# Kernel tuning notes

Hardware: AMD Instinct MI355X
Metric: run time of the kernel (lower is better)

## Reference

```python
import jax, jax.numpy as jnp
import numpy as np

B, N, C, H = 8, 16384, 256, 128
FG_NPOINT = 4096
SAMPLE_POINT = 1024
MAX_TRANSLATE = jnp.array([3.0, 3.0, 2.0], dtype=jnp.float32)


def _fps(xyz, n_sample):
    # xyz: [N,3] -> indices [n_sample] (D-FPS, seed index 0)
    d0 = jnp.sum((xyz - xyz[0]) ** 2, axis=-1)  # [N]

    def body(dists, _):
        idx = jnp.argmax(dists)
        d = jnp.sum((xyz - xyz[idx]) ** 2, axis=-1)
        return jnp.minimum(dists, d), idx

    _, idxs = jax.lax.scan(body, d0, None, length=n_sample - 1)
    return jnp.concatenate([jnp.zeros((1,), dtype=idxs.dtype), idxs])


def fps_batch(xyz, n_sample):
    return jax.vmap(lambda p: _fps(p, n_sample))(xyz)  # [B, n_sample]


def gather_pts(xyz, idx):
    # xyz [B,N,3], idx [B,S] -> [B,S,3]
    return jnp.take_along_axis(xyz, idx[..., None], axis=1)


def gather_feat(feat, idx):
    # feat [B,C,N], idx [B,S] -> [B,C,S]
    return jnp.take_along_axis(feat, idx[:, None, :], axis=2)


def setup_inputs() -> dict:
    key = jax.random.key(0)
    ks = jax.random.split(key, 6)
    return {
        "xyz": jax.random.normal(ks[0], (B, N, 3), jnp.float32) * 10.0,
        "features": jax.random.normal(ks[1], (B, C, N), jnp.float32),
        "seg_w1": jax.random.normal(ks[2], (H, C), jnp.float32) * 0.05,
        "seg_scale1": jnp.ones((H,), jnp.float32),
        "seg_bias1": jnp.zeros((H,), jnp.float32),
        "seg_w2": jax.random.normal(ks[3], (1, H), jnp.float32) * 0.05,
        "seg_b2": jnp.zeros((1,), jnp.float32),
        "vote_w1": jax.random.normal(ks[4], (H, C), jnp.float32) * 0.05,
        "vote_scale1": jnp.ones((H,), jnp.float32),
        "vote_bias1": jnp.zeros((H,), jnp.float32),
        "reg_w": jax.random.normal(ks[5], (3, H), jnp.float32) * 0.05,
        "reg_b": jnp.zeros((3,), jnp.float32),
    }


def reference(xyz, features, seg_w1, seg_scale1, seg_bias1, seg_w2, seg_b2,
              vote_w1, vote_scale1, vote_bias1, reg_w, reg_b):
    # ---- seg branch: 1x1 conv + BN(eval affine) + ReLU, then 1x1 conv to num_class
    h = jax.nn.relu(jnp.einsum('oc,bcn->bon', seg_w1, features)
                    * seg_scale1[None, :, None] + seg_bias1[None, :, None])
    seg = jnp.einsum('oc,bon->bcn'.replace('c', 'k'), seg_w2, h)  # [B,1,N]
    seg = seg + seg_b2[None, :, None]
    seg_score = jax.nn.sigmoid(jnp.max(seg, axis=1))  # [B,N] (max over class dim)

    # ---- top-k foreground selection
    _, fg_idx = jax.lax.top_k(seg_score, FG_NPOINT)  # [B,M]
    fg_xyz = gather_pts(xyz, fg_idx)                  # [B,M,3]
    fg_feat = gather_feat(features, fg_idx)           # [B,C,M]

    # ---- vote/offset layer (3DSSD-style): MLP -> clamped offset
    vh = jax.nn.relu(jnp.einsum('oc,bcm->bom', vote_w1, fg_feat)
                     * vote_scale1[None, :, None] + vote_bias1[None, :, None])  # [B,H,M]
    reg = jnp.einsum('oh,bhm->bom', reg_w, vh) + reg_b[None, :, None]  # [B,3,M]
    offset = jnp.clip(reg.transpose(0, 2, 1), -MAX_TRANSLATE, MAX_TRANSLATE)  # [B,M,3]
    fg_xyz_ctr = fg_xyz + offset
    fg_feat_ctr = vh

    # ---- original-point FPS sampler + gathers
    ori_idx = fps_batch(fg_xyz, SAMPLE_POINT)
    sampled_ori_xyz = gather_pts(fg_xyz, ori_idx)
    sampled_ori_feat = gather_feat(fg_feat, ori_idx)

    # ---- center-point FPS sampler + gathers
    ctr_idx = fps_batch(fg_xyz_ctr, SAMPLE_POINT)
    sampled_ctr_xyz = gather_pts(fg_xyz_ctr, ctr_idx)
    sampled_ctr_feat = gather_feat(fg_feat_ctr, ctr_idx)
    sampled_ctr_offset = gather_pts(offset, ctr_idx)
    sampled_ctr_origin = gather_pts(fg_xyz, ctr_idx)

    # ---- aggregation concat (USE_ORIGINAL_POINT=True)
    agg_xyz = jnp.concatenate([sampled_ctr_xyz, sampled_ori_xyz], axis=1)       # [B,2S,3]
    agg_feat = jnp.concatenate([sampled_ctr_feat, sampled_ori_feat[:, :H, :]], axis=-1)  # [B,H,2S]

    return (agg_xyz, agg_feat, sampled_ctr_xyz, sampled_ctr_offset,
            sampled_ctr_origin, seg)
```

## Files before the change

kernel.cpp:

```cpp
#include <hip/hip_runtime.h>

#define NB 8
#define NP 16384
#define NC 256
#define NH 128
#define NM 4096
#define NS 1024

typedef float v2f __attribute__((ext_vector_type(2)));

__device__ __forceinline__ unsigned long long make_key(float v, int n) {
  unsigned u = __float_as_uint(v);
  u = (u & 0x80000000u) ? ~u : (u | 0x80000000u);
  unsigned d = ~u;
  return (((unsigned long long)d) << 32) | (unsigned)n;
}

__device__ __forceinline__ float wave_max_dpp(float v) {
#define DPPMAX(ctrl)                                                            \
  v = fmaxf(v, __int_as_float(__builtin_amdgcn_update_dpp(                      \
                 __float_as_int(v), __float_as_int(v), (ctrl), 0xf, 0xf, false)))
  DPPMAX(0xB1);
  DPPMAX(0x4E);
  DPPMAX(0x141);
  DPPMAX(0x140);
  DPPMAX(0x142);
  DPPMAX(0x143);
#undef DPPMAX
  return __int_as_float(__builtin_amdgcn_readlane(__float_as_int(v), 63));
}

template <int CTRL>
__device__ __forceinline__ unsigned long long dpp64(unsigned long long v) {
  int lo = (int)(unsigned)v, hi = (int)(unsigned)(v >> 32);
  lo = __builtin_amdgcn_update_dpp(lo, lo, CTRL, 0xf, 0xf, false);
  hi = __builtin_amdgcn_update_dpp(hi, hi, CTRL, 0xf, 0xf, false);
  return (((unsigned long long)(unsigned)hi) << 32) | (unsigned)lo;
}

__global__ __launch_bounds__(256) void transpose_w_kernel(
    const float* __restrict__ wseg, const float* __restrict__ wvote,
    float* __restrict__ tseg, float* __restrict__ tvote) {
  int i = blockIdx.x * 256 + threadIdx.x;
  int c = i >> 7, o = i & 127;
  tseg[i] = wseg[o * NC + c];
  tvote[i] = wvote[o * NC + c];
}

__global__ __launch_bounds__(256) void seg_kernel(
    const float* __restrict__ features, const float* __restrict__ w1t,
    const float* __restrict__ scale1, const float* __restrict__ bias1,
    const float* __restrict__ w2, const float* __restrict__ b2,
    float* __restrict__ seg_out, unsigned long long* __restrict__ keys) {
  __shared__ float wt[32][128];
  __shared__ float ft[32][64];
  __shared__ float red[16][64];
  __shared__ float Ssh[64];
  __shared__ float w2sh[128];
  int b = blockIdx.y;
  int n0 = blockIdx.x * 64;
  int tid = threadIdx.x;
  int lane = tid & 63;
  int ro = tid >> 4, rc = tid & 15;
  float a0 = w2[lane], a1 = w2[lane + 64];
  float whi = fmaxf(a0, a1), wlo = fminf(a0, a1);
#pragma unroll
  for (int off = 32; off >= 1; off >>= 1) {
    whi = fmaxf(whi, __shfl_xor(whi, off, 64));
    wlo = fminf(wlo, __shfl_xor(wlo, off, 64));
  }
  if (tid < 128) w2sh[tid] = w2[tid];
  const float* fb = features + (size_t)b * NC * NP;
  float acc[8][4] = {};
  for (int kc = 0; kc < NC; kc += 32) {
    for (int q = tid; q < 4096; q += 256) {
      int kk = q >> 7, o = q & 127;
      wt[kk][o] = w1t[(kc + kk) * NH + o];
    }
    for (int q = tid; q < 2048; q += 256) {
      int kk = q >> 6, nn = q & 63;
      ft[kk][nn] = fb[(size_t)(kc + kk) * NP + n0 + nn];
    }
    __syncthreads();
#pragma unroll
    for (int kk = 0; kk < 32; ++kk) {
      float wv[8], fv[4];
#pragma unroll
      for (int i = 0; i < 8; ++i) wv[i] = wt[kk][ro * 8 + i];
#pragma unroll
      for (int j = 0; j < 4; ++j) fv[j] = ft[kk][rc * 4 + j];
#pragma unroll
      for (int i = 0; i < 8; ++i)
#pragma unroll
        for (int j = 0; j < 4; ++j) acc[i][j] = fmaf(wv[i], fv[j], acc[i][j]);
    }
    __syncthreads();
  }
  float part[4] = {};
#pragma unroll
  for (int i = 0; i < 8; ++i) {
    int o = ro * 8 + i;
    float sc = scale1[o], bi = bias1[o];
#pragma unroll
    for (int j = 0; j < 4; ++j) {
      float h = fmaxf(fmaf(acc[i][j], sc, bi), 0.0f);
      part[j] += h;
    }
  }
#pragma unroll
  for (int j = 0; j < 4; ++j) red[ro][rc * 4 + j] = part[j];
  __syncthreads();
  float b2v = b2[0];
  if (tid < 64) {
    float S = 0.0f;
#pragma unroll
    for (int r = 0; r < 16; ++r) S += red[r][tid];
    Ssh[tid] = S;
    float m = (S >= 0.0f ? whi * S : wlo * S) + b2v;
    float sig = 1.0f / (1.0f + expf(-m));
    int nn = n0 + tid;
    keys[(size_t)b * NP + nn] = make_key(sig, nn);
  }
  __syncthreads();
  int n = tid & 63, kg = tid >> 6;
  float S = Ssh[n];
  size_t base = ((size_t)b * 128 + (size_t)kg * 32) * NP + n0 + n;
#pragma unroll
  for (int kk = 0; kk < 32; ++kk)
    seg_out[base + (size_t)kk * NP] = fmaf(w2sh[kg * 32 + kk], S, b2v);
}

__global__ __launch_bounds__(1024) void sort8k_kernel(unsigned long long* __restrict__ keys) {
  __shared__ unsigned long long sk[8192];
  int chunk = blockIdx.x & 1, b = blockIdx.x >> 1;
  bool desc = (chunk == 1);
  unsigned long long* K = keys + (size_t)b * NP + chunk * 8192;
  int tid = threadIdx.x;
  for (int i = tid; i < 8192; i += 1024) sk[i] = K[i];
  __syncthreads();
  for (int k = 2; k <= 8192; k <<= 1) {
    for (int j = k >> 1; j > 0; j >>= 1) {
      for (int i = tid; i < 8192; i += 1024) {
        int ixj = i ^ j;
        if (ixj > i) {
          bool up = (((i & k) == 0) != desc);
          unsigned long long a = sk[i], c = sk[ixj];
          if ((a > c) == up) { sk[i] = c; sk[ixj] = a; }
        }
      }
      __syncthreads();
    }
  }
  for (int i = tid; i < 8192; i += 1024) K[i] = sk[i];
}

__global__ __launch_bounds__(1024) void merge_topk_kernel(
    const unsigned long long* __restrict__ keys, int* __restrict__ fg_idx,
    float* __restrict__ fg_xyz, const float* __restrict__ xyz) {
  __shared__ unsigned long long sk[8192];
  int b = blockIdx.x;
  const unsigned long long* K = keys + (size_t)b * NP;
  int tid = threadIdx.x;
  for (int i = tid; i < 8192; i += 1024) {
    unsigned long long a = K[i], c = K[i + 8192];
    sk[i] = (a < c) ? a : c;
  }
  __syncthreads();
  for (int j = 4096; j > 0; j >>= 1) {
    for (int i = tid; i < 8192; i += 1024) {
      int ixj = i ^ j;
      if (ixj > i) {
        unsigned long long a = sk[i], c = sk[ixj];
        if (a > c) { sk[i] = c; sk[ixj] = a; }
      }
    }
    __syncthreads();
  }
  for (int m = tid; m < NM; m += 1024) {
    unsigned long long key = sk[m];
    int idx = (int)(key & 0xffffffffULL);
    fg_idx[b * NM + m] = idx;
    size_t src = ((size_t)b * NP + idx) * 3;
    size_t dst = ((size_t)b * NM + m) * 3;
    fg_xyz[dst + 0] = xyz[src + 0];
    fg_xyz[dst + 1] = xyz[src + 1];
    fg_xyz[dst + 2] = xyz[src + 2];
  }
}

__global__ __launch_bounds__(256) void vote_kernel(
    const float* __restrict__ features, const int* __restrict__ fg_idx,
    const float* __restrict__ w1t, const float* __restrict__ scale1,
    const float* __restrict__ bias1, const float* __restrict__ rw,
    const float* __restrict__ rb, const float* __restrict__ fg_xyz,
    float* __restrict__ vh, float* __restrict__ offs, float* __restrict__ fg_ctr) {
  __shared__ float wt[32][128];
  __shared__ float ft[32][64];
  __shared__ float hl[128][65];
  __shared__ int idx_l[64];
  int b = blockIdx.y;
  int m0 = blockIdx.x * 64;
  int tid = threadIdx.x;
  int ro = tid >> 4, rc = tid & 15;
  const float* fb = features + (size_t)b * NC * NP;
  if (tid < 64) idx_l[tid] = fg_idx[b * NM + m0 + tid];
  __syncthreads();
  float acc[8][4] = {};
  for (int kc = 0; kc < NC; kc += 32) {
    for (int q = tid; q < 4096; q += 256) {
      int kk = q >> 7, o = q & 127;
      wt[kk][o] = w1t[(kc + kk) * NH + o];
    }
    for (int q = tid; q < 2048; q += 256) {
      int kk = q >> 6, mm = q & 63;
      ft[kk][mm] = fb[(size_t)(kc + kk) * NP + idx_l[mm]];
    }
    __syncthreads();
#pragma unroll
    for (int kk = 0; kk < 32; ++kk) {
      float wv[8], fv[4];
#pragma unroll
      for (int i = 0; i < 8; ++i) wv[i] = wt[kk][ro * 8 + i];
#pragma unroll
      for (int j = 0; j < 4; ++j) fv[j] = ft[kk][rc * 4 + j];
#pragma unroll
      for (int i = 0; i < 8; ++i)
#pragma unroll
        for (int j = 0; j < 4; ++j) acc[i][j] = fmaf(wv[i], fv[j], acc[i][j]);
    }
    __syncthreads();
  }
#pragma unroll
  for (int i = 0; i < 8; ++i) {
    int o = ro * 8 + i;
    float sc = scale1[o], bi = bias1[o];
#pragma unroll
    for (int j = 0; j < 4; ++j) {
      float h = fmaxf(fmaf(acc[i][j], sc, bi), 0.0f);
      hl[o][rc * 4 + j] = h;
      vh[((size_t)b * NH + o) * NM + m0 + rc * 4 + j] = h;
    }
  }
  __syncthreads();
  if (tid < 64) {
    int m = m0 + tid;
    const float MT[3] = {3.0f, 3.0f, 2.0f};
#pragma unroll
    for (int r = 0; r < 3; ++r) {
      float a = 0.0f;
      for (int o = 0; o < NH; ++o) a = fmaf(rw[r * NH + o], hl[o][tid], a);
      a += rb[r];
      a = fminf(fmaxf(a, -MT[r]), MT[r]);
      size_t p = ((size_t)b * NM + m) * 3 + r;
      offs[p] = a;
      fg_ctr[p] = __fadd_rn(fg_xyz[p], a);
    }
  }
}

#define PPT 8
__global__ __launch_bounds__(512) void fps_kernel(
    const float* __restrict__ fg_xyz, const float* __restrict__ fg_ctr,
    int* __restrict__ ori_idx, int* __restrict__ ctr_idx) {
#pragma clang fp contract(off)
  __shared__ float4 pts[NM];
  __shared__ unsigned long long wkey[2][8];
  __shared__ int sel_list[NS];
  int set = blockIdx.x & 1, b = blockIdx.x >> 1;
  const float* P = (set == 0 ? fg_xyz : fg_ctr) + (size_t)b * NM * 3;
  int* O = (set == 0 ? ori_idx : ctr_idx) + b * NS;
  int tid = threadIdx.x;
  for (int m = tid; m < NM; m += 512)
    pts[m] = make_float4(P[m * 3 + 0], P[m * 3 + 1], P[m * 3 + 2], 0.0f);
  __syncthreads();
  v2f x2[4], y2[4], z2[4], d2[4];
#pragma unroll
  for (int j = 0; j < 4; ++j) {
    float4 pa = pts[tid * PPT + 2 * j];
    float4 pb = pts[tid * PPT + 2 * j + 1];
    v2f t;
    t.x = pa.x; t.y = pb.x; x2[j] = t;
    t.x = pa.y; t.y = pb.y; y2[j] = t;
    t.x = pa.z; t.y = pb.z; z2[j] = t;
    t.x = 3.402823466e38f; t.y = 3.402823466e38f; d2[j] = t;
  }
  if (tid == 0) sel_list[0] = 0;
  int lane = tid & 63, wave = tid >> 6;
  int base_idx = tid * PPT;
  float sx = pts[0].x, sy = pts[0].y, sz = pts[0].z;
  for (int it = 1; it < NS; ++it) {
    v2f sxv, syv, szv;
    sxv.x = sx; sxv.y = sx;
    syv.x = sy; syv.y = sy;
    szv.x = sz; szv.y = sz;
    float bd = -1.0f;
    int bc = 0;
#pragma unroll
    for (int j = 0; j < 4; ++j) {
      v2f dx = x2[j] - sxv, dy = y2[j] - syv, dz = z2[j] - szv;
      v2f dd = (dx * dx + dy * dy) + dz * dz;
      v2f nd;
      nd.x = fminf(d2[j].x, dd.x);
      nd.y = fminf(d2[j].y, dd.y);
      d2[j] = nd;
      if (j == 0) {
        bd = nd.x; bc = base_idx;
        bool g = nd.y > bd; bd = g ? nd.y : bd; bc = g ? base_idx + 1 : bc;
      } else {
        bool g0 = nd.x > bd; bd = g0 ? nd.x : bd; bc = g0 ? base_idx + 2 * j : bc;
        bool g1 = nd.y > bd; bd = g1 ? nd.y : bd; bc = g1 ? base_idx + 2 * j + 1 : bc;
      }
    }
    float wm = wave_max_dpp(bd);
    unsigned long long msk = __ballot(bd == wm);
    int wl = __ffsll((long long)msk) - 1;
    if (lane == wl)
      wkey[it & 1][wave] =
          (((unsigned long long)__float_as_uint(bd)) << 32) | (unsigned)(4095 - bc);
    __syncthreads();
    unsigned long long k = wkey[it & 1][lane & 7];
    { unsigned long long o = dpp64<0xB1>(k);  if (o > k) k = o; }
    { unsigned long long o = dpp64<0x4E>(k);  if (o > k) k = o; }
    { unsigned long long o = dpp64<0x141>(k); if (o > k) k = o; }
    int sel = 4095 - (int)(k & 0xffffffffULL);
    if (tid == 0) sel_list[it] = sel;
    float4 s = pts[sel];
    sx = s.x; sy = s.y; sz = s.z;
  }
  __syncthreads();
  for (int s2 = tid; s2 < NS; s2 += 512) O[s2] = sel_list[s2];
}

__global__ __launch_bounds__(256) void feat_out_kernel(
    const float* __restrict__ vh, const float* __restrict__ features,
    const int* __restrict__ fg_idx, const int* __restrict__ ori_idx,
    const int* __restrict__ ctr_idx, float* __restrict__ out_feat) {
  int b = blockIdx.z;
  int o = blockIdx.y * 4 + (threadIdx.x >> 6);
  int s = blockIdx.x * 64 + (threadIdx.x & 63);
  float val;
  if (s < NS) {
    int i = ctr_idx[b * NS + s];
    val = vh[((size_t)b * NH + o) * NM + i];
  } else {
    int i = ori_idx[b * NS + (s - NS)];
    int g = fg_idx[b * NM + i];
    val = features[((size_t)b * NC + o) * NP + g];
  }
  out_feat[((size_t)b * NH + o) * (2 * NS) + s] = val;
}

__global__ __launch_bounds__(256) void xyz_out_kernel(
    const float* __restrict__ fg_xyz, const float* __restrict__ fg_ctr,
    const float* __restrict__ offs, const int* __restrict__ ori_idx,
    const int* __restrict__ ctr_idx, float* __restrict__ out_agg,
    float* __restrict__ out_cxyz, float* __restrict__ out_coff,
    float* __restrict__ out_corg) {
  int b = blockIdx.y;
  int s = blockIdx.x * 256 + threadIdx.x;
  if (s < NS) {
    int i = ctr_idx[b * NS + s];
    size_t src = ((size_t)b * NM + i) * 3;
    size_t d_agg = ((size_t)b * 2 * NS + s) * 3;
    size_t d_s = ((size_t)b * NS + s) * 3;
#pragma unroll
    for (int r = 0; r < 3; ++r) {
      float c = fg_ctr[src + r];
      out_agg[d_agg + r] = c;
      out_cxyz[d_s + r] = c;
      out_coff[d_s + r] = offs[src + r];
      out_corg[d_s + r] = fg_xyz[src + r];
    }
  } else {
    int i = ori_idx[b * NS + (s - NS)];
    size_t src = ((size_t)b * NM + i) * 3;
    size_t d_agg = ((size_t)b * 2 * NS + s) * 3;
#pragma unroll
    for (int r = 0; r < 3; ++r) out_agg[d_agg + r] = fg_xyz[src + r];
  }
}

extern "C" void kernel_launch(void* const* d_in, const int* in_sizes, int n_in,
                              void* d_out, int out_size, void* d_ws, size_t ws_size,
                              hipStream_t stream) {
  const float* xyz = (const float*)d_in[0];
  const float* features = (const float*)d_in[1];
  const float* seg_w1 = (const float*)d_in[2];
  const float* seg_scale1 = (const float*)d_in[3];
  const float* seg_bias1 = (const float*)d_in[4];
  const float* seg_w2 = (const float*)d_in[5];
  const float* seg_b2 = (const float*)d_in[6];
  const float* vote_w1 = (const float*)d_in[7];
  const float* vote_scale1 = (const float*)d_in[8];
  const float* vote_bias1 = (const float*)d_in[9];
  const float* reg_w = (const float*)d_in[10];
  const float* reg_b = (const float*)d_in[11];
  float* out = (float*)d_out;

  char* ws = (char*)d_ws;
  unsigned long long* keys = (unsigned long long*)(ws + 0);
  int* fg_idx = (int*)(ws + 1048576);
  float* fg_xyz = (float*)(ws + 1179648);
  float* fg_ctr = (float*)(ws + 1572864);
  float* offs = (float*)(ws + 1966080);
  int* ori_idx = (int*)(ws + 2359296);
  int* ctr_idx = (int*)(ws + 2392064);
  float* vh = (float*)(ws + 2424832);
  float* w1t_s = (float*)(ws + 19202048);
  float* w1t_v = (float*)(ws + 19333120);

  float* out_agg_xyz = out;
  float* out_agg_feat = out + 49152;
  float* out_ctr_xyz = out + 2146304;
  float* out_ctr_off = out + 2170880;
  float* out_ctr_org = out + 2195456;
  float* out_seg = out + 2220032;

  transpose_w_kernel<<<128, 256, 0, stream>>>(seg_w1, vote_w1, w1t_s, w1t_v);
  seg_kernel<<<dim3(NP / 64, NB), 256, 0, stream>>>(
      features, w1t_s, seg_scale1, seg_bias1, seg_w2, seg_b2, out_seg, keys);
  sort8k_kernel<<<2 * NB, 1024, 0, stream>>>(keys);
  merge_topk_kernel<<<NB, 1024, 0, stream>>>(keys, fg_idx, fg_xyz, xyz);
  vote_kernel<<<dim3(NM / 64, NB), 256, 0, stream>>>(
      features, fg_idx, w1t_v, vote_scale1, vote_bias1, reg_w, reg_b, fg_xyz,
      vh, offs, fg_ctr);
  fps_kernel<<<16, 512, 0, stream>>>(fg_xyz, fg_ctr, ori_idx, ctr_idx);
  feat_out_kernel<<<dim3(32, 32, NB), 256, 0, stream>>>(
      vh, features, fg_idx, ori_idx, ctr_idx, out_agg_feat);
  xyz_out_kernel<<<dim3(8, NB), 256, 0, stream>>>(
      fg_xyz, fg_ctr, offs, ori_idx, ctr_idx, out_agg_xyz, out_ctr_xyz,
      out_ctr_off, out_ctr_org);
}
```

Baseline: 1.083 ms.

## Fuse both FPS samplers per batch into one block sharing barriers

The FPS kernel now runs the original-point and center-point samplers for one batch inside a single block, interleaving the two per-iteration updates so they share one __syncthreads per iteration. This halves the block count (8 instead of 16) and amortizes barrier and reduction latency across two independent chains. Point storage moves from float4 AoS to SoA arrays, and indices are written directly to global instead of buffered in shared memory. It doubles per-thread register use and leaves more of the GPU idle, so the serial per-iteration cost must drop enough to compensate.

```diff
diff --git a/kernel.cpp b/kernel.cpp
--- a/kernel.cpp
+++ b/kernel.cpp
@@ -259,76 +259,103 @@
 }
 
 #define PPT 8
+__device__ __forceinline__ void fps_update8(
+    const v2f* x, const v2f* y, const v2f* z, v2f* d,
+    float sx, float sy, float sz, int base_idx, float& bd, int& bc) {
+#pragma clang fp contract(off)
+  v2f sxv, syv, szv;
+  sxv.x = sx; sxv.y = sx;
+  syv.x = sy; syv.y = sy;
+  szv.x = sz; szv.y = sz;
+  bd = -1.0f;
+  bc = base_idx;
+#pragma unroll
+  for (int j = 0; j < 4; ++j) {
+    v2f dx = x[j] - sxv, dy = y[j] - syv, dz = z[j] - szv;
+    v2f dd = (dx * dx + dy * dy) + dz * dz;
+    v2f nd;
+    nd.x = fminf(d[j].x, dd.x);
+    nd.y = fminf(d[j].y, dd.y);
+    d[j] = nd;
+    if (j == 0) {
+      bd = nd.x; bc = base_idx;
+      bool g = nd.y > bd; bd = g ? nd.y : bd; bc = g ? base_idx + 1 : bc;
+    } else {
+      bool g0 = nd.x > bd; bd = g0 ? nd.x : bd; bc = g0 ? base_idx + 2 * j : bc;
+      bool g1 = nd.y > bd; bd = g1 ? nd.y : bd; bc = g1 ? base_idx + 2 * j + 1 : bc;
+    }
+  }
+}
+
 __global__ __launch_bounds__(512) void fps_kernel(
     const float* __restrict__ fg_xyz, const float* __restrict__ fg_ctr,
     int* __restrict__ ori_idx, int* __restrict__ ctr_idx) {
 #pragma clang fp contract(off)
-  __shared__ float4 pts[NM];
-  __shared__ unsigned long long wkey[2][8];
-  __shared__ int sel_list[NS];
-  int set = blockIdx.x & 1, b = blockIdx.x >> 1;
-  const float* P = (set == 0 ? fg_xyz : fg_ctr) + (size_t)b * NM * 3;
-  int* O = (set == 0 ? ori_idx : ctr_idx) + b * NS;
+  __shared__ float pxA[NM], pyA[NM], pzA[NM];
+  __shared__ float pxB[NM], pyB[NM], pzB[NM];
+  __shared__ unsigned long long wkeyA[2][8], wkeyB[2][8];
+  int b = blockIdx.x;
+  const float* PA = fg_xyz + (size_t)b * NM * 3;
+  const float* PB = fg_ctr + (size_t)b * NM * 3;
+  int* OA = ori_idx + b * NS;
+  int* OB = ctr_idx + b * NS;
   int tid = threadIdx.x;
-  for (int m = tid; m < NM; m += 512)
-    pts[m] = make_float4(P[m * 3 + 0], P[m * 3 + 1], P[m * 3 + 2], 0.0f);
-  __syncthreads();
-  v2f x2[4], y2[4], z2[4], d2[4];
+  for (int m = tid; m < NM; m += 512) {
+    pxA[m] = PA[m * 3 + 0]; pyA[m] = PA[m * 3 + 1]; pzA[m] = PA[m * 3 + 2];
+    pxB[m] = PB[m * 3 + 0]; pyB[m] = PB[m * 3 + 1]; pzB[m] = PB[m * 3 + 2];
+  }
+  __syncthreads();
+  v2f xA[4], yA[4], zA[4], dA[4], xB[4], yB[4], zB[4], dB[4];
+  int base_idx = tid * PPT;
 #pragma unroll
   for (int j = 0; j < 4; ++j) {
-    float4 pa = pts[tid * PPT + 2 * j];
-    float4 pb = pts[tid * PPT + 2 * j + 1];
+    int m0 = base_idx + 2 * j, m1 = m0 + 1;
     v2f t;
-    t.x = pa.x; t.y = pb.x; x2[j] = t;
-    t.x = pa.y; t.y = pb.y; y2[j] = t;
-    t.x = pa.z; t.y = pb.z; z2[j] = t;
-    t.x = 3.402823466e38f; t.y = 3.402823466e38f; d2[j] = t;
-  }
-  if (tid == 0) sel_list[0] = 0;
+    t.x = pxA[m0]; t.y = pxA[m1]; xA[j] = t;
+    t.x = pyA[m0]; t.y = pyA[m1]; yA[j] = t;
+    t.x = pzA[m0]; t.y = pzA[m1]; zA[j] = t;
+    t.x = pxB[m0]; t.y = pxB[m1]; xB[j] = t;
+    t.x = pyB[m0]; t.y = pyB[m1]; yB[j] = t;
+    t.x = pzB[m0]; t.y = pzB[m1]; zB[j] = t;
+    t.x = 3.402823466e38f; t.y = 3.402823466e38f;
+    dA[j] = t; dB[j] = t;
+  }
+  if (tid == 0) { OA[0] = 0; OB[0] = 0; }
   int lane = tid & 63, wave = tid >> 6;
-  int base_idx = tid * PPT;
-  float sx = pts[0].x, sy = pts[0].y, sz = pts[0].z;
+  float sxA = pxA[0], syA = pyA[0], szA = pzA[0];
+  float sxB = pxB[0], syB = pyB[0], szB = pzB[0];
   for (int it = 1; it < NS; ++it) {
-    v2f sxv, syv, szv;
-    sxv.x = sx; sxv.y = sx;
-    syv.x = sy; syv.y = sy;
-    szv.x = sz; szv.y = sz;
-    float bd = -1.0f;
-    int bc = 0;
-#pragma unroll
-    for (int j = 0; j < 4; ++j) {
-      v2f dx = x2[j] - sxv, dy = y2[j] - syv, dz = z2[j] - szv;
-      v2f dd = (dx * dx + dy * dy) + dz * dz;
-      v2f nd;
-      nd.x = fminf(d2[j].x, dd.x);
-      nd.y = fminf(d2[j].y, dd.y);
-      d2[j] = nd;
-      if (j == 0) {
-        bd = nd.x; bc = base_idx;
-        bool g = nd.y > bd; bd = g ? nd.y : bd; bc = g ? base_idx + 1 : bc;
-      } else {
-        bool g0 = nd.x > bd; bd = g0 ? nd.x : bd; bc = g0 ? base_idx + 2 * j : bc;
-        bool g1 = nd.y > bd; bd = g1 ? nd.y : bd; bc = g1 ? base_idx + 2 * j + 1 : bc;
-      }
-    }
-    float wm = wave_max_dpp(bd);
-    unsigned long long msk = __ballot(bd == wm);
-    int wl = __ffsll((long long)msk) - 1;
-    if (lane == wl)
-      wkey[it & 1][wave] =
-          (((unsigned long long)__float_as_uint(bd)) << 32) | (unsigned)(4095 - bc);
-    __syncthreads();
-    unsigned long long k = wkey[it & 1][lane & 7];
-    { unsigned long long o = dpp64<0xB1>(k);  if (o > k) k = o; }
-    { unsigned long long o = dpp64<0x4E>(k);  if (o > k) k = o; }
-    { unsigned long long o = dpp64<0x141>(k); if (o > k) k = o; }
-    int sel = 4095 - (int)(k & 0xffffffffULL);
-    if (tid == 0) sel_list[it] = sel;
-    float4 s = pts[sel];
-    sx = s.x; sy = s.y; sz = s.z;
-  }
-  __syncthreads();
-  for (int s2 = tid; s2 < NS; s2 += 512) O[s2] = sel_list[s2];
+    float bdA; int bcA;
+    fps_update8(xA, yA, zA, dA, sxA, syA, szA, base_idx, bdA, bcA);
+    float wmA = wave_max_dpp(bdA);
+    unsigned long long mA = __ballot(bdA == wmA);
+    int wlA = __ffsll((long long)mA) - 1;
+    if (lane == wlA)
+      wkeyA[it & 1][wave] =
+          (((unsigned long long)__float_as_uint(bdA)) << 32) | (unsigned)(4095 - bcA);
+    float bdB; int bcB;
+    fps_update8(xB, yB, zB, dB, sxB, syB, szB, base_idx, bdB, bcB);
+    float wmB = wave_max_dpp(bdB);
+    unsigned long long mB = __ballot(bdB == wmB);
+    int wlB = __ffsll((long long)mB) - 1;
+    if (lane == wlB)
+      wkeyB[it & 1][wave] =
+          (((unsigned long long)__float_as_uint(bdB)) << 32) | (unsigned)(4095 - bcB);
+    __syncthreads();
+    unsigned long long kA = wkeyA[it & 1][lane & 7];
+    unsigned long long kB = wkeyB[it & 1][lane & 7];
+    { unsigned long long o = dpp64<0xB1>(kA);  if (o > kA) kA = o; }
+    { unsigned long long o = dpp64<0xB1>(kB);  if (o > kB) kB = o; }
+    { unsigned long long o = dpp64<0x4E>(kA);  if (o > kA) kA = o; }
+    { unsigned long long o = dpp64<0x4E>(kB);  if (o > kB) kB = o; }
+    { unsigned long long o = dpp64<0x141>(kA); if (o > kA) kA = o; }
+    { unsigned long long o = dpp64<0x141>(kB); if (o > kB) kB = o; }
+    int selA = 4095 - (int)(kA & 0xffffffffULL);
+    int selB = 4095 - (int)(kB & 0xffffffffULL);
+    if (tid == 0) { OA[it] = selA; OB[it] = selB; }
+    sxA = pxA[selA]; syA = pyA[selA]; szA = pzA[selA];
+    sxB = pxB[selB]; syB = pyB[selB]; szB = pzB[selB];
+  }
 }
 
 __global__ __launch_bounds__(256) void feat_out_kernel(
@@ -424,7 +451,7 @@
   vote_kernel<<<dim3(NM / 64, NB), 256, 0, stream>>>(
       features, fg_idx, w1t_v, vote_scale1, vote_bias1, reg_w, reg_b, fg_xyz,
       vh, offs, fg_ctr);
-  fps_kernel<<<16, 512, 0, stream>>>(fg_xyz, fg_ctr, ori_idx, ctr_idx);
+  fps_kernel<<<NB, 512, 0, stream>>>(fg_xyz, fg_ctr, ori_idx, ctr_idx);
   feat_out_kernel<<<dim3(32, 32, NB), 256, 0, stream>>>(
       vh, features, fg_idx, ori_idx, ctr_idx, out_agg_feat);
   xyz_out_kernel<<<dim3(8, NB), 256, 0, stream>>>(
```

New measurement: 1.531 ms. +41.4%, slower.

## Merge both FPS samplers per batch into one 1024-thread block with SoA LDS

Applied to the files above, without the earlier changes.

Each block now runs the original-point and center-point FPS for one batch at once, using two 512-thread groups that share a single barrier per iteration, instead of launching 16 separate 512-thread blocks. Point coordinates move from float4 AoS to SoA shared arrays, and the selected indices go straight to global memory rather than through a shared list. This halves the block count and combines the per-iteration barrier traffic. The risk is that 1024-thread barriers are slower than 512-thread ones and that 8 blocks use fewer CUs.

```diff
diff --git a/kernel.cpp b/kernel.cpp
--- a/kernel.cpp
+++ b/kernel.cpp
@@ -259,76 +259,85 @@
 }
 
 #define PPT 8
-__global__ __launch_bounds__(512) void fps_kernel(
+__device__ __forceinline__ void fps_update8(
+    const v2f* x, const v2f* y, const v2f* z, v2f* d,
+    float sx, float sy, float sz, int base_idx, float& bd, int& bc) {
+#pragma clang fp contract(off)
+  v2f sxv, syv, szv;
+  sxv.x = sx; sxv.y = sx;
+  syv.x = sy; syv.y = sy;
+  szv.x = sz; szv.y = sz;
+  bd = -1.0f;
+  bc = base_idx;
+#pragma unroll
+  for (int j = 0; j < 4; ++j) {
+    v2f dx = x[j] - sxv, dy = y[j] - syv, dz = z[j] - szv;
+    v2f dd = (dx * dx + dy * dy) + dz * dz;
+    v2f nd;
+    nd.x = fminf(d[j].x, dd.x);
+    nd.y = fminf(d[j].y, dd.y);
+    d[j] = nd;
+    if (j == 0) {
+      bd = nd.x; bc = base_idx;
+      bool g = nd.y > bd; bd = g ? nd.y : bd; bc = g ? base_idx + 1 : bc;
+    } else {
+      bool g0 = nd.x > bd; bd = g0 ? nd.x : bd; bc = g0 ? base_idx + 2 * j : bc;
+      bool g1 = nd.y > bd; bd = g1 ? nd.y : bd; bc = g1 ? base_idx + 2 * j + 1 : bc;
+    }
+  }
+}
+
+__global__ __launch_bounds__(1024) void fps_kernel(
     const float* __restrict__ fg_xyz, const float* __restrict__ fg_ctr,
     int* __restrict__ ori_idx, int* __restrict__ ctr_idx) {
 #pragma clang fp contract(off)
-  __shared__ float4 pts[NM];
-  __shared__ unsigned long long wkey[2][8];
-  __shared__ int sel_list[NS];
-  int set = blockIdx.x & 1, b = blockIdx.x >> 1;
-  const float* P = (set == 0 ? fg_xyz : fg_ctr) + (size_t)b * NM * 3;
-  int* O = (set == 0 ? ori_idx : ctr_idx) + b * NS;
+  __shared__ float px[2][NM], py[2][NM], pz[2][NM];
+  __shared__ unsigned long long wkey[2][2][8];
+  int b = blockIdx.x;
   int tid = threadIdx.x;
-  for (int m = tid; m < NM; m += 512)
-    pts[m] = make_float4(P[m * 3 + 0], P[m * 3 + 1], P[m * 3 + 2], 0.0f);
+  int grp = tid >> 9;
+  int ltid = tid & 511;
+  const float* P = (grp == 0 ? fg_xyz : fg_ctr) + (size_t)b * NM * 3;
+  int* O = (grp == 0 ? ori_idx : ctr_idx) + b * NS;
+  for (int m = ltid; m < NM; m += 512) {
+    px[grp][m] = P[m * 3 + 0];
+    py[grp][m] = P[m * 3 + 1];
+    pz[grp][m] = P[m * 3 + 2];
+  }
   __syncthreads();
   v2f x2[4], y2[4], z2[4], d2[4];
+  int base_idx = ltid * PPT;
 #pragma unroll
   for (int j = 0; j < 4; ++j) {
-    float4 pa = pts[tid * PPT + 2 * j];
-    float4 pb = pts[tid * PPT + 2 * j + 1];
+    int m0 = base_idx + 2 * j, m1 = m0 + 1;
     v2f t;
-    t.x = pa.x; t.y = pb.x; x2[j] = t;
-    t.x = pa.y; t.y = pb.y; y2[j] = t;
-    t.x = pa.z; t.y = pb.z; z2[j] = t;
-    t.x = 3.402823466e38f; t.y = 3.402823466e38f; d2[j] = t;
-  }
-  if (tid == 0) sel_list[0] = 0;
-  int lane = tid & 63, wave = tid >> 6;
-  int base_idx = tid * PPT;
-  float sx = pts[0].x, sy = pts[0].y, sz = pts[0].z;
+    t.x = px[grp][m0]; t.y = px[grp][m1]; x2[j] = t;
+    t.x = py[grp][m0]; t.y = py[grp][m1]; y2[j] = t;
+    t.x = pz[grp][m0]; t.y = pz[grp][m1]; z2[j] = t;
+    t.x = 3.402823466e38f; t.y = 3.402823466e38f;
+    d2[j] = t;
+  }
+  if (ltid == 0) O[0] = 0;
+  int lane = tid & 63, gwave = (tid >> 6) & 7;
+  float sx = px[grp][0], sy = py[grp][0], sz = pz[grp][0];
   for (int it = 1; it < NS; ++it) {
-    v2f sxv, syv, szv;
-    sxv.x = sx; sxv.y = sx;
-    syv.x = sy; syv.y = sy;
-    szv.x = sz; szv.y = sz;
-    float bd = -1.0f;
-    int bc = 0;
-#pragma unroll
-    for (int j = 0; j < 4; ++j) {
-      v2f dx = x2[j] - sxv, dy = y2[j] - syv, dz = z2[j] - szv;
-      v2f dd = (dx * dx + dy * dy) + dz * dz;
-      v2f nd;
-      nd.x = fminf(d2[j].x, dd.x);
-      nd.y = fminf(d2[j].y, dd.y);
-      d2[j] = nd;
-      if (j == 0) {
-        bd = nd.x; bc = base_idx;
-        bool g = nd.y > bd; bd = g ? nd.y : bd; bc = g ? base_idx + 1 : bc;
-      } else {
-        bool g0 = nd.x > bd; bd = g0 ? nd.x : bd; bc = g0 ? base_idx + 2 * j : bc;
-        bool g1 = nd.y > bd; bd = g1 ? nd.y : bd; bc = g1 ? base_idx + 2 * j + 1 : bc;
-      }
-    }
+    float bd; int bc;
+    fps_update8(x2, y2, z2, d2, sx, sy, sz, base_idx, bd, bc);
     float wm = wave_max_dpp(bd);
     unsigned long long msk = __ballot(bd == wm);
     int wl = __ffsll((long long)msk) - 1;
     if (lane == wl)
-      wkey[it & 1][wave] =
+      wkey[grp][it & 1][gwave] =
           (((unsigned long long)__float_as_uint(bd)) << 32) | (unsigned)(4095 - bc);
     __syncthreads();
-    unsigned long long k = wkey[it & 1][lane & 7];
+    unsigned long long k = wkey[grp][it & 1][lane & 7];
     { unsigned long long o = dpp64<0xB1>(k);  if (o > k) k = o; }
     { unsigned long long o = dpp64<0x4E>(k);  if (o > k) k = o; }
     { unsigned long long o = dpp64<0x141>(k); if (o > k) k = o; }
     int sel = 4095 - (int)(k & 0xffffffffULL);
-    if (tid == 0) sel_list[it] = sel;
-    float4 s = pts[sel];
-    sx = s.x; sy = s.y; sz = s.z;
-  }
-  __syncthreads();
-  for (int s2 = tid; s2 < NS; s2 += 512) O[s2] = sel_list[s2];
+    if (ltid == 0) O[it] = sel;
+    sx = px[grp][sel]; sy = py[grp][sel]; sz = pz[grp][sel];
+  }
 }
 
 __global__ __launch_bounds__(256) void feat_out_kernel(
@@ -424,7 +433,7 @@
   vote_kernel<<<dim3(NM / 64, NB), 256, 0, stream>>>(
       features, fg_idx, w1t_v, vote_scale1, vote_bias1, reg_w, reg_b, fg_xyz,
       vh, offs, fg_ctr);
-  fps_kernel<<<16, 512, 0, stream>>>(fg_xyz, fg_ctr, ori_idx, ctr_idx);
+  fps_kernel<<<NB, 1024, 0, stream>>>(fg_xyz, fg_ctr, ori_idx, ctr_idx);
   feat_out_kernel<<<dim3(32, 32, NB), 256, 0, stream>>>(
       vh, features, fg_idx, ori_idx, ctr_idx, out_agg_feat);
   xyz_out_kernel<<<dim3(8, NB), 256, 0, stream>>>(
```

Result: slower. 1.430 ms (+32.0%).

## Halve FPS block to four waves, 16 points per thread, simpler cross-wave reduction

Applied to the files above, without the earlier changes.

The FPS kernel now runs 256 threads per block instead of 512, with each thread holding 16 points in registers. The cross-wave argmax becomes two 128-bit shared loads plus scalar max compares, replacing the DPP shuffle over 8 wave keys. Point storage moves from float4 AoS to separate x/y/z arrays in shared memory. The aim is to cut barrier and reduction latency in the serial 1023-iteration loop, at the cost of twice the per-thread distance work and higher register pressure.

```diff
diff --git a/kernel.cpp b/kernel.cpp
--- a/kernel.cpp
+++ b/kernel.cpp
@@ -28,14 +28,6 @@
   DPPMAX(0x143);
 #undef DPPMAX
   return __int_as_float(__builtin_amdgcn_readlane(__float_as_int(v), 63));
-}
-
-template <int CTRL>
-__device__ __forceinline__ unsigned long long dpp64(unsigned long long v) {
-  int lo = (int)(unsigned)v, hi = (int)(unsigned)(v >> 32);
-  lo = __builtin_amdgcn_update_dpp(lo, lo, CTRL, 0xf, 0xf, false);
-  hi = __builtin_amdgcn_update_dpp(hi, hi, CTRL, 0xf, 0xf, false);
-  return (((unsigned long long)(unsigned)hi) << 32) | (unsigned)lo;
 }
 
 __global__ __launch_bounds__(256) void transpose_w_kernel(
@@ -258,45 +250,48 @@
   }
 }
 
-#define PPT 8
-__global__ __launch_bounds__(512) void fps_kernel(
+#define PPT 16
+__global__ __launch_bounds__(256) void fps_kernel(
     const float* __restrict__ fg_xyz, const float* __restrict__ fg_ctr,
     int* __restrict__ ori_idx, int* __restrict__ ctr_idx) {
 #pragma clang fp contract(off)
-  __shared__ float4 pts[NM];
-  __shared__ unsigned long long wkey[2][8];
+  __shared__ float px[NM], py[NM], pz[NM];
+  __shared__ __align__(32) unsigned long long wkey[2][4];
   __shared__ int sel_list[NS];
   int set = blockIdx.x & 1, b = blockIdx.x >> 1;
   const float* P = (set == 0 ? fg_xyz : fg_ctr) + (size_t)b * NM * 3;
   int* O = (set == 0 ? ori_idx : ctr_idx) + b * NS;
   int tid = threadIdx.x;
-  for (int m = tid; m < NM; m += 512)
-    pts[m] = make_float4(P[m * 3 + 0], P[m * 3 + 1], P[m * 3 + 2], 0.0f);
-  __syncthreads();
-  v2f x2[4], y2[4], z2[4], d2[4];
-#pragma unroll
-  for (int j = 0; j < 4; ++j) {
-    float4 pa = pts[tid * PPT + 2 * j];
-    float4 pb = pts[tid * PPT + 2 * j + 1];
+  for (int m = tid; m < NM; m += 256) {
+    px[m] = P[m * 3 + 0];
+    py[m] = P[m * 3 + 1];
+    pz[m] = P[m * 3 + 2];
+  }
+  __syncthreads();
+  v2f x2[8], y2[8], z2[8], d2[8];
+  int base_idx = tid * PPT;
+#pragma unroll
+  for (int j = 0; j < 8; ++j) {
+    int m0 = base_idx + 2 * j, m1 = m0 + 1;
     v2f t;
-    t.x = pa.x; t.y = pb.x; x2[j] = t;
-    t.x = pa.y; t.y = pb.y; y2[j] = t;
-    t.x = pa.z; t.y = pb.z; z2[j] = t;
-    t.x = 3.402823466e38f; t.y = 3.402823466e38f; d2[j] = t;
+    t.x = px[m0]; t.y = px[m1]; x2[j] = t;
+    t.x = py[m0]; t.y = py[m1]; y2[j] = t;
+    t.x = pz[m0]; t.y = pz[m1]; z2[j] = t;
+    t.x = 3.402823466e38f; t.y = 3.402823466e38f;
+    d2[j] = t;
   }
   if (tid == 0) sel_list[0] = 0;
   int lane = tid & 63, wave = tid >> 6;
-  int base_idx = tid * PPT;
-  float sx = pts[0].x, sy = pts[0].y, sz = pts[0].z;
+  float sx = px[0], sy = py[0], sz = pz[0];
   for (int it = 1; it < NS; ++it) {
     v2f sxv, syv, szv;
     sxv.x = sx; sxv.y = sx;
     syv.x = sy; syv.y = sy;
     szv.x = sz; szv.y = sz;
     float bd = -1.0f;
-    int bc = 0;
-#pragma unroll
-    for (int j = 0; j < 4; ++j) {
+    int bc = base_idx;
+#pragma unroll
+    for (int j = 0; j < 8; ++j) {
       v2f dx = x2[j] - sxv, dy = y2[j] - syv, dz = z2[j] - szv;
       v2f dd = (dx * dx + dy * dy) + dz * dz;
       v2f nd;
@@ -318,17 +313,17 @@
       wkey[it & 1][wave] =
           (((unsigned long long)__float_as_uint(bd)) << 32) | (unsigned)(4095 - bc);
     __syncthreads();
-    unsigned long long k = wkey[it & 1][lane & 7];
-    { unsigned long long o = dpp64<0xB1>(k);  if (o > k) k = o; }
-    { unsigned long long o = dpp64<0x4E>(k);  if (o > k) k = o; }
-    { unsigned long long o = dpp64<0x141>(k); if (o > k) k = o; }
-    int sel = 4095 - (int)(k & 0xffffffffULL);
+    const ulonglong2* wk = (const ulonglong2*)&wkey[it & 1][0];
+    ulonglong2 q0 = wk[0], q1 = wk[1];
+    unsigned long long m0 = q0.x > q0.y ? q0.x : q0.y;
+    unsigned long long m1 = q1.x > q1.y ? q1.x : q1.y;
+    unsigned long long km = m0 > m1 ? m0 : m1;
+    int sel = 4095 - (int)(km & 0xffffffffULL);
     if (tid == 0) sel_list[it] = sel;
-    float4 s = pts[sel];
-    sx = s.x; sy = s.y; sz = s.z;
-  }
-  __syncthreads();
-  for (int s2 = tid; s2 < NS; s2 += 512) O[s2] = sel_list[s2];
+    sx = px[sel]; sy = py[sel]; sz = pz[sel];
+  }
+  __syncthreads();
+  for (int s2 = tid; s2 < NS; s2 += 256) O[s2] = sel_list[s2];
 }
 
 __global__ __launch_bounds__(256) void feat_out_kernel(
@@ -424,7 +419,7 @@
   vote_kernel<<<dim3(NM / 64, NB), 256, 0, stream>>>(
       features, fg_idx, w1t_v, vote_scale1, vote_bias1, reg_w, reg_b, fg_xyz,
       vh, offs, fg_ctr);
-  fps_kernel<<<16, 512, 0, stream>>>(fg_xyz, fg_ctr, ori_idx, ctr_idx);
+  fps_kernel<<<16, 256, 0, stream>>>(fg_xyz, fg_ctr, ori_idx, ctr_idx);
   feat_out_kernel<<<dim3(32, 32, NB), 256, 0, stream>>>(
       vh, features, fg_idx, ori_idx, ctr_idx, out_agg_feat);
   xyz_out_kernel<<<dim3(8, NB), 256, 0, stream>>>(
```

Measured after the change: 997.2 us. -7.9%, faster.
